# Performance work log

Hardware: AMD Instinct MI355X
Metric: run time of the kernel (lower is better)

Reference implementation:

```python
import jax, jax.numpy as jnp
import numpy as np

N_NODES = 100000
N_EDGES = 1600000
EMB = 128
N_LAYER = 5
X_DIM = 178
E_DIM = 18
BN_EPS = 1e-5


def setup_inputs() -> dict:
    key = jax.random.key(0)
    ks = jax.random.split(key, 20)
    s = 0.05  # weight scale
    inp = {}
    inp["x"] = jax.random.normal(ks[0], (N_NODES, X_DIM), jnp.float32)
    inp["edge_attr"] = jax.random.uniform(ks[1], (N_EDGES, E_DIM), jnp.float32)
    # input MLP (178 -> emb -> emb, LeakyReLU 0.1)
    inp["iw1"] = jax.random.normal(ks[2], (X_DIM, EMB), jnp.float32) * s
    inp["ib1"] = jax.random.normal(ks[3], (EMB,), jnp.float32) * s
    inp["iw2"] = jax.random.normal(ks[4], (EMB, EMB), jnp.float32) * s
    inp["ib2"] = jax.random.normal(ks[5], (EMB,), jnp.float32) * s
    # per-layer edge embedding MLP (18 -> emb -> emb, LeakyReLU 0.1)
    inp["ew1"] = jax.random.normal(ks[6], (N_LAYER, E_DIM, EMB), jnp.float32) * s
    inp["eb1"] = jax.random.normal(ks[7], (N_LAYER, EMB), jnp.float32) * s
    inp["ew2"] = jax.random.normal(ks[8], (N_LAYER, EMB, EMB), jnp.float32) * s
    inp["eb2"] = jax.random.normal(ks[9], (N_LAYER, EMB), jnp.float32) * s
    # per-layer GIN update MLP (emb -> 2emb -> emb, ReLU)
    inp["mw1"] = jax.random.normal(ks[10], (N_LAYER, EMB, 2 * EMB), jnp.float32) * s
    inp["mb1"] = jax.random.normal(ks[11], (N_LAYER, 2 * EMB), jnp.float32) * s
    inp["mw2"] = jax.random.normal(ks[12], (N_LAYER, 2 * EMB, EMB), jnp.float32) * s
    inp["mb2"] = jax.random.normal(ks[13], (N_LAYER, EMB), jnp.float32) * s
    # per-layer BatchNorm affine params
    inp["gamma"] = jnp.ones((N_LAYER, EMB), jnp.float32)
    inp["beta"] = jnp.zeros((N_LAYER, EMB), jnp.float32)
    inp["edge_index"] = jax.random.randint(ks[14], (2, N_EDGES), 0, N_NODES)
    return inp


def _leaky(v):
    return jnp.where(v > 0, v, 0.1 * v)


def reference(x, edge_attr, iw1, ib1, iw2, ib2, ew1, eb1, ew2, eb2,
              mw1, mb1, mw2, mb2, gamma, beta, edge_index):
    src = edge_index[0]  # x_j gathered from source nodes (PyG source_to_target)
    dst = edge_index[1]
    n = x.shape[0]

    # input node MLP with LeakyReLU(0.1)
    h = _leaky(x @ iw1 + ib1) @ iw2 + ib2  # [N, EMB]

    for l in range(N_LAYER):
        # edge embeddings for real edges: [E, EMB]
        ee = _leaky(edge_attr @ ew1[l] + eb1[l]) @ ew2[l] + eb2[l]
        # self-loop edges have zero edge_attr -> constant embedding vector [EMB]
        self_e = _leaky(eb1[l]) @ ew2[l] + eb2[l]
        # message = x_j + edge_emb; aggregate (add) at destination, plus self-loop term
        msg = h[src] + ee
        aggr = jax.ops.segment_sum(msg, dst, num_segments=n) + h + self_e
        # GIN update MLP (ReLU)
        hh = jnp.maximum(aggr @ mw1[l] + mb1[l], 0.0) @ mw2[l] + mb2[l]
        # BatchNorm1d (training mode: batch stats, biased variance)
        mean = hh.mean(axis=0)
        var = hh.var(axis=0)
        hh = (hh - mean) / jnp.sqrt(var + BN_EPS) * gamma[l] + beta[l]
        if l < N_LAYER - 1:
            hh = jnp.maximum(hh, 0.0)  # ReLU on all but last layer; dropout p=0 is a no-op
        h = hh

    return h  # JK == 'last'
```

## Files before the change

kernel.cpp:

```cpp
#include <hip/hip_runtime.h>
#include <hip/hip_bf16.h>
#include <cstdint>
#include <cstddef>

#define NNODES 100000
#define NEDGES 1600000
#define EMBD 128
#define NLAYER 5
#define XDIM 178
#define EDIM 18
#define BNEPS 1e-5f

typedef __attribute__((ext_vector_type(8))) short short8;
typedef __attribute__((ext_vector_type(8))) unsigned short ushort8;
typedef __attribute__((ext_vector_type(4))) float f32x4;

static __device__ __forceinline__ float leakyf(float v){ return v > 0.f ? v : 0.1f*v; }
static __device__ __forceinline__ unsigned short f2b(float v){
  __hip_bfloat16 b = __float2bfloat16(v);
  return *reinterpret_cast<unsigned short*>(&b);
}
static __device__ __forceinline__ float b2f(unsigned short u){
  __hip_bfloat16 b = *reinterpret_cast<__hip_bfloat16*>(&u);
  return __bfloat162float(b);
}

__global__ __launch_bounds__(256) void k_hist(const int* __restrict__ dst, int* __restrict__ cnt){
  int e = blockIdx.x*256 + threadIdx.x;
  if (e < NEDGES) atomicAdd(&cnt[dst[e]], 1);
}

__global__ __launch_bounds__(256) void k_scan1(const int* __restrict__ cnt, int* __restrict__ rowptr,
                                               int* __restrict__ bsum){
  __shared__ int s[256];
  int t = threadIdx.x, i = blockIdx.x*256 + t;
  int v = (i < NNODES) ? cnt[i] : 0;
  s[t] = v; __syncthreads();
  for (int off=1; off<256; off<<=1){
    int x = (t>=off) ? s[t-off] : 0; __syncthreads();
    s[t] += x; __syncthreads();
  }
  if (i < NNODES) rowptr[i+1] = s[t];
  if (t == 255) bsum[blockIdx.x] = s[t];
}

__global__ __launch_bounds__(512) void k_scan2(const int* __restrict__ bsum, int* __restrict__ boff, int nb){
  __shared__ int s[512];
  int t = threadIdx.x;
  int v = (t < nb) ? bsum[t] : 0;
  s[t] = v; __syncthreads();
  for (int off=1; off<512; off<<=1){
    int x = (t>=off) ? s[t-off] : 0; __syncthreads();
    s[t] += x; __syncthreads();
  }
  if (t < nb) boff[t] = s[t] - v;
}

__global__ __launch_bounds__(256) void k_scan3(int* __restrict__ rowptr, const int* __restrict__ boff){
  int i = blockIdx.x*256 + threadIdx.x;
  if (i < NNODES) rowptr[i+1] += boff[i>>8];
  if (i == 0) rowptr[0] = 0;
}

__global__ __launch_bounds__(256) void k_curcopy(const int* __restrict__ rowptr, int* __restrict__ cursor){
  int i = blockIdx.x*256 + threadIdx.x;
  if (i < NNODES) cursor[i] = rowptr[i];
}

__global__ __launch_bounds__(256) void k_fill_new(const int* __restrict__ src, const int* __restrict__ dst,
                                                  const float* __restrict__ ea, int* __restrict__ cursor,
                                                  int* __restrict__ srcp, unsigned short* __restrict__ eap24){
  int e = blockIdx.x*256 + threadIdx.x;
  if (e >= NEDGES) return;
  int pos = atomicAdd(&cursor[dst[e]], 1);
  srcp[pos] = src[e];
  const float* a = ea + (size_t)e*EDIM;
  ushort8 r0, r1, r2;
  #pragma unroll
  for (int k=0;k<8;++k)  r0[k] = f2b(a[k]);
  #pragma unroll
  for (int k=0;k<8;++k)  r1[k] = f2b(a[8+k]);
  #pragma unroll
  for (int k=0;k<8;++k)  r2[k] = 0;
  r2[0] = f2b(a[16]); r2[1] = f2b(a[17]);
  r2[2] = 0x3F80;
  unsigned short* o = eap24 + (size_t)pos*24;
  *reinterpret_cast<ushort8*>(o)      = r0;
  *reinterpret_cast<ushort8*>(o + 8)  = r1;
  *reinterpret_cast<ushort8*>(o + 16) = r2;
}

__global__ __launch_bounds__(256) void k_fill(const int* __restrict__ src, const int* __restrict__ dst,
                                              const float* __restrict__ ea, int* __restrict__ cursor,
                                              int* __restrict__ perm, int* __restrict__ srcp,
                                              float* __restrict__ eap){
  int e = blockIdx.x*256 + threadIdx.x;
  if (e >= NEDGES) return;
  int pos = atomicAdd(&cursor[dst[e]], 1);
  perm[pos] = e;
  srcp[pos] = src[e];
  if (eap){
    const float* a = ea + (size_t)e*EDIM;
    float* o = eap + (size_t)pos*EDIM;
    #pragma unroll
    for (int k=0;k<EDIM;++k) o[k] = a[k];
  }
}

__global__ __launch_bounds__(128) void k_selfe(const float* __restrict__ eb1, const float* __restrict__ ew2,
                                               const float* __restrict__ eb2, float* __restrict__ selfe){
  int l = blockIdx.x, c = threadIdx.x;
  const float* b1 = eb1 + l*EMBD;
  const float* w2 = ew2 + (size_t)l*EMBD*EMBD;
  float acc = eb2[l*EMBD + c];
  for (int j=0;j<EMBD;++j) acc += leakyf(b1[j]) * w2[j*EMBD + c];
  selfe[l*EMBD + c] = acc;
}

__global__ __launch_bounds__(256) void k_wc(const float* __restrict__ ew2, const float* __restrict__ mw1,
                                            float* __restrict__ wc){
  int idx = blockIdx.x*256 + threadIdx.x;
  int l = idx >> 15, rem = idx & 32767;
  int i = rem >> 8, n = rem & 255;
  const float* e = ew2 + (size_t)l*EMBD*EMBD + i*EMBD;
  const float* m = mw1 + (size_t)l*EMBD*2*EMBD + n;
  float acc = 0.f;
  #pragma unroll 4
  for (int j=0;j<EMBD;++j) acc += e[j]*m[(size_t)j*2*EMBD];
  wc[idx] = acc;
}

__global__ __launch_bounds__(256) void k_pack(const float* __restrict__ s1, int rows1,
                                              const float* __restrict__ s2, int Kreal,
                                              int Kpad, int N, __hip_bfloat16* __restrict__ out){
  int idx = blockIdx.x*256 + threadIdx.x;
  if (idx >= Kpad*N) return;
  int k = idx / N, n = idx - k*N;
  float v = 0.f;
  if (k < rows1) v = s1[(size_t)k*N + n];
  else if (k < Kreal) v = s2[(size_t)(k-rows1)*N + n];
  unsigned short hi = f2b(v);
  unsigned short lo = f2b(v - b2f(hi));
  size_t o = (size_t)(k>>5)*N*32 + (size_t)n*32 + (k&31);
  unsigned short* po = (unsigned short*)out;
  po[o] = hi;
  po[(size_t)Kpad*N + o] = lo;
}

__global__ __launch_bounds__(256) void k_edge_mfma(
    const float* __restrict__ h, const int* __restrict__ rowptr,
    const int* __restrict__ srcp, const unsigned short* __restrict__ eap24,
    const float* __restrict__ ew1l, const float* __restrict__ eb1l,
    const float* __restrict__ eb2l, const float* __restrict__ selfel,
    float* __restrict__ S1, float* __restrict__ base)
{
  int tid = threadIdx.x;
  int lane = tid & 63;
  int lr = lane & 15, kb = lane >> 4;
  int half = lane >> 5, li = lane & 31;
  int c4 = li*4;

  short8 bh[8], bl[8];
  #pragma unroll
  for (int nf=0; nf<8; ++nf){
    int col = nf*16 + lr;
    ushort8 hh8, ll8;
    #pragma unroll
    for (int j=0;j<8;++j){
      int k = kb*8 + j;
      float v = 0.f;
      if (k < EDIM) v = ew1l[k*EMBD + col];
      else if (k == EDIM) v = eb1l[col];
      unsigned short hi = f2b(v);
      hh8[j] = hi;
      ll8[j] = f2b(v - b2f(hi));
    }
    bh[nf] = *reinterpret_cast<short8*>(&hh8);
    bl[nf] = *reinterpret_cast<short8*>(&ll8);
  }
  float4 sf4 = *(const float4*)(selfel + c4);
  float4 e24 = *(const float4*)(eb2l + c4);

  int wid = blockIdx.x*4 + (tid>>6);
  const int NW = gridDim.x*4;
  for (int node = wid; node < NNODES; node += NW){
    int rs = rowptr[node], re = rowptr[node+1];
    float s1p[8];
    #pragma unroll
    for (int nf=0;nf<8;++nf) s1p[nf]=0.f;
    f32x4 bacc = (f32x4)0.f;

    for (int c0 = rs; c0 < re; c0 += 16){
      int cnt = re - c0;

      #pragma unroll
      for (int p=0;p<8;++p){
        int r = 2*p + half;
        int e = c0 + r; if (e > re-1) e = re-1;
        float m = (r < cnt) ? 1.f : 0.f;
        int sp = srcp[e];
        float4 hv = *(const float4*)(h + (size_t)sp*EMBD + c4);
        bacc[0] = fmaf(m, hv.x, bacc[0]);
        bacc[1] = fmaf(m, hv.y, bacc[1]);
        bacc[2] = fmaf(m, hv.z, bacc[2]);
        bacc[3] = fmaf(m, hv.w, bacc[3]);
      }

      int idx = c0 + lr; if (idx > re-1) idx = re-1;
      short8 af = (short8)0;
      if (kb < 3){
        ushort8 t = *reinterpret_cast<const ushort8*>(eap24 + (size_t)idx*24 + kb*8);
        af = *reinterpret_cast<short8*>(&t);
      }
      if (lr >= cnt) af = (short8)0;
      #pragma unroll
      for (int nf=0;nf<8;++nf){
        f32x4 acc = (f32x4)0.f;
        acc = __builtin_amdgcn_mfma_f32_16x16x32_bf16(af, bl[nf], acc, 0,0,0);
        acc = __builtin_amdgcn_mfma_f32_16x16x32_bf16(af, bh[nf], acc, 0,0,0);
        #pragma unroll
        for (int j=0;j<4;++j){
          float v = acc[j];
          s1p[nf] = fmaf(0.55f, v, s1p[nf]);
          s1p[nf] = fmaf(0.45f, fabsf(v), s1p[nf]);
        }
      }
    }

    #pragma unroll
    for (int nf=0;nf<8;++nf){
      float v = s1p[nf];
      v += __shfl_xor(v, 16);
      v += __shfl_xor(v, 32);
      s1p[nf] = v;
    }
    float va = s1p[0], vb = s1p[1];
    if (kb == 1){ va = s1p[2]; vb = s1p[3]; }
    if (kb == 2){ va = s1p[4]; vb = s1p[5]; }
    if (kb == 3){ va = s1p[6]; vb = s1p[7]; }
    S1[(size_t)node*EMBD + kb*32 + lr]      = va;
    S1[(size_t)node*EMBD + kb*32 + 16 + lr] = vb;

    #pragma unroll
    for (int j=0;j<4;++j) bacc[j] += __shfl_xor(bacc[j], 32);

    if (half == 0){
      float deg = (float)(re - rs);
      float4 hn = *(const float4*)(h + (size_t)node*EMBD + c4);
      float4 o;
      o.x = bacc[0] + hn.x + sf4.x + deg*e24.x;
      o.y = bacc[1] + hn.y + sf4.y + deg*e24.y;
      o.z = bacc[2] + hn.z + sf4.z + deg*e24.z;
      o.w = bacc[3] + hn.w + sf4.w + deg*e24.w;
      *(float4*)(base + (size_t)node*EMBD + c4) = o;
    }
  }
}

__global__ __launch_bounds__(256) void k_edge(
    const float* __restrict__ h, const int* __restrict__ rowptr,
    const int* __restrict__ perm, const int* __restrict__ srcp,
    const float* __restrict__ edge_attr, const float* __restrict__ eaperm,
    const float* __restrict__ ew1l, const float* __restrict__ eb1l,
    const float* __restrict__ eb2l, const float* __restrict__ selfel,
    float* __restrict__ S1, float* __restrict__ base)
{
  __shared__ float w1s[EDIM*EMBD];
  __shared__ float b1s[EMBD];
  int tid = threadIdx.x;
  for (int i = tid; i < EDIM*EMBD; i += 256) w1s[i] = ew1l[i];
  if (tid < EMBD) b1s[tid] = eb1l[tid];
  __syncthreads();
  int lane = tid & 63;
  int node = blockIdx.x*4 + (tid >> 6);
  if (node >= NNODES) return;
  int rs = rowptr[node], re = rowptr[node+1];
  int c0 = lane*2;
  float s1x=0.f, s1y=0.f, bx=0.f, by=0.f;
  for (int i = rs; i < re; ++i){
    int s = __builtin_amdgcn_readfirstlane(srcp[i]);
    const float* ea;
    if (eaperm){
      ea = eaperm + (size_t)__builtin_amdgcn_readfirstlane(i)*EDIM;
    } else {
      ea = edge_attr + (size_t)__builtin_amdgcn_readfirstlane(perm[i])*EDIM;
    }
    float2 hs = *(const float2*)(h + (size_t)s*EMBD + c0);
    bx += hs.x; by += hs.y;
    float d0 = b1s[c0], d1 = b1s[c0+1];
    #pragma unroll
    for (int k=0;k<EDIM;++k){
      float av = ea[k];
      d0 += av * w1s[k*EMBD + c0];
      d1 += av * w1s[k*EMBD + c0 + 1];
    }
    s1x += leakyf(d0); s1y += leakyf(d1);
  }
  float deg = (float)(re - rs);
  float2 hv = *(const float2*)(h + (size_t)node*EMBD + c0);
  *(float2*)(S1 + (size_t)node*EMBD + c0) = make_float2(s1x, s1y);
  float bvx = bx + hv.x + selfel[c0]   + deg*eb2l[c0];
  float bvy = by + hv.y + selfel[c0+1] + deg*eb2l[c0+1];
  *(float2*)(base + (size_t)node*EMBD + c0) = make_float2(bvx, bvy);
}

template<int BN, int WGM, int WGN, bool ALO, int ACT, bool STATS, bool OBF16, bool CONCAT, bool KCHK, bool ABF16>
__global__ __launch_bounds__(512) void k_mgemm(
    const float* __restrict__ Af, const float* __restrict__ A1,
    const __hip_bfloat16* __restrict__ Ab,
    int M, int Kreal, int Kpad, int lda,
    const __hip_bfloat16* __restrict__ Bp,
    const float* __restrict__ bias,
    float* __restrict__ Cf, __hip_bfloat16* __restrict__ Cb, int ldc,
    float* __restrict__ stats)
{
  static_assert(WGM*WGN == 8, "8 waves");
  constexpr int BM = 128;
  constexpr int MF = BM/(16*WGM);
  constexpr int NF = BN/(16*WGN);
  constexpr int LDS_ROW = 40;
  __shared__ __align__(16) unsigned short Ah[BM*LDS_ROW];
  __shared__ __align__(16) unsigned short Al[ALO ? BM*LDS_ROW : 8];
  __shared__ float ssum[STATS ? BN : 4];
  __shared__ float ssq [STATS ? BN : 4];

  int tid = threadIdx.x;
  int row0 = blockIdx.x*BM;
  int w = tid >> 6, lane = tid & 63;
  int wm = w / WGN, wn = w % WGN;
  int lr = lane & 15, kb = lane >> 4;
  int wrow = wm*MF*16, wcol = wn*NF*16;

  if (STATS && tid < BN){ ssum[tid] = 0.f; ssq[tid] = 0.f; }

  f32x4 acc[MF][NF];
  #pragma unroll
  for (int a=0;a<MF;++a)
    #pragma unroll
    for (int b=0;b<NF;++b) acc[a][b] = (f32x4)0.f;

  const size_t planeSz = (size_t)Kpad*BN;
  int sr = tid >> 2;
  int skq = (tid & 3)*8;
  int grow = row0 + sr;
  const int KS = Kpad >> 5;

  for (int ks = 0; ks < KS; ++ks){
    int k0 = ks << 5;
    int kg = k0 + skq;
    ushort8 hv, lv;
    if (ABF16){
      short8 raw = (short8)0;
      if (grow < M) raw = *reinterpret_cast<const short8*>((const unsigned short*)Ab + (size_t)grow*lda + kg);
      hv = *reinterpret_cast<ushort8*>(&raw);
    } else {
      float v[8];
      if (KCHK){
        #pragma unroll
        for (int i=0;i<8;++i)
          v[i] = (grow < M && kg+i < Kreal) ? Af[(size_t)grow*lda + kg + i] : 0.f;
      } else {
        const float* s;
        if (CONCAT) s = (kg < EMBD) ? (Af + (size_t)grow*lda + kg) : (A1 + (size_t)grow*lda + (kg - EMBD));
        else        s = Af + (size_t)grow*lda + kg;
        float4 p0 = make_float4(0,0,0,0), p1 = make_float4(0,0,0,0);
        if (grow < M){ p0 = *(const float4*)s; p1 = *(const float4*)(s+4); }
        v[0]=p0.x; v[1]=p0.y; v[2]=p0.z; v[3]=p0.w;
        v[4]=p1.x; v[5]=p1.y; v[6]=p1.z; v[7]=p1.w;
      }
      #pragma unroll
      for (int i=0;i<8;++i){
        unsigned short h16 = f2b(v[i]);
        hv[i] = h16;
        if (ALO) lv[i] = f2b(v[i] - b2f(h16));
      }
    }
    __syncthreads();
    *reinterpret_cast<ushort8*>(&Ah[sr*LDS_ROW + skq]) = hv;
    if (ALO && !ABF16) *reinterpret_cast<ushort8*>(&Al[sr*LDS_ROW + skq]) = lv;
    __syncthreads();

    short8 ah[MF], al[MF];
    #pragma unroll
    for (int mf=0; mf<MF; ++mf){
      int r = (wrow + mf*16 + lr)*LDS_ROW + kb*8;
      ah[mf] = *reinterpret_cast<const short8*>(&Ah[r]);
      if (ALO) al[mf] = *reinterpret_cast<const short8*>(&Al[r]);
    }
    const unsigned short* bb = (const unsigned short*)Bp + (size_t)ks*BN*32;
    short8 bh[NF], blv[NF];
    #pragma unroll
    for (int nf=0; nf<NF; ++nf){
      size_t off = (size_t)(wcol + nf*16 + lr)*32 + kb*8;
      bh[nf] = *reinterpret_cast<const short8*>(bb + off);
      blv[nf] = *reinterpret_cast<const short8*>(bb + planeSz + off);
    }
    #pragma unroll
    for (int mf=0; mf<MF; ++mf){
      #pragma unroll
      for (int nf=0; nf<NF; ++nf){
        acc[mf][nf] = __builtin_amdgcn_mfma_f32_16x16x32_bf16(ah[mf], bh[nf], acc[mf][nf], 0, 0, 0);
        acc[mf][nf] = __builtin_amdgcn_mfma_f32_16x16x32_bf16(ah[mf], blv[nf], acc[mf][nf], 0, 0, 0);
        if (ALO)
          acc[mf][nf] = __builtin_amdgcn_mfma_f32_16x16x32_bf16(al[mf], bh[nf], acc[mf][nf], 0, 0, 0);
      }
    }
  }

  float bcol[NF];
  #pragma unroll
  for (int nf=0; nf<NF; ++nf) bcol[nf] = bias ? bias[wcol + nf*16 + lr] : 0.f;
  float s[NF], sq[NF];
  #pragma unroll
  for (int nf=0; nf<NF; ++nf){ s[nf]=0.f; sq[nf]=0.f; }

  #pragma unroll
  for (int mf=0; mf<MF; ++mf){
    #pragma unroll
    for (int j=0; j<4; ++j){
      int r = row0 + wrow + mf*16 + kb*4 + j;
      if (r < M){
        #pragma unroll
        for (int nf=0; nf<NF; ++nf){
          int c = wcol + nf*16 + lr;
          float v = acc[mf][nf][j] + bcol[nf];
          if (ACT == 1) v = leakyf(v);
          if (ACT == 2) v = fmaxf(v, 0.f);
          if (OBF16) Cb[(size_t)r*ldc + c] = __float2bfloat16(v);
          else       Cf[(size_t)r*ldc + c] = v;
          if (STATS){ s[nf] += v; sq[nf] += v*v; }
        }
      }
    }
  }
  if (STATS){
    #pragma unroll
    for (int nf=0; nf<NF; ++nf){
      atomicAdd(&ssum[wcol + nf*16 + lr], s[nf]);
      atomicAdd(&ssq [wcol + nf*16 + lr], sq[nf]);
    }
    __syncthreads();
    if (tid < BN){
      atomicAdd(&stats[tid], ssum[tid]);
      atomicAdd(&stats[BN + tid], ssq[tid]);
    }
  }
}

__global__ __launch_bounds__(256) void k_bn(const float* __restrict__ hh, const float* __restrict__ stats,
                                            const float* __restrict__ gamma, const float* __restrict__ beta,
                                            float* __restrict__ out, int dorelu){
  int idx = blockIdx.x*256 + threadIdx.x;
  if (idx >= NNODES*(EMBD/4)) return;
  int c0 = (idx & (EMBD/4 - 1)) * 4;
  float4 v = *(const float4*)(hh + (size_t)idx*4);
  float o[4] = {v.x, v.y, v.z, v.w};
  const float invN = 1.f / (float)NNODES;
  #pragma unroll
  for (int i=0;i<4;++i){
    int c = c0 + i;
    float mean = stats[c] * invN;
    float var  = stats[EMBD + c] * invN - mean*mean;
    float inv  = rsqrtf(fmaxf(var, 0.f) + BNEPS);
    float y = (o[i] - mean) * inv * gamma[c] + beta[c];
    if (dorelu) y = fmaxf(y, 0.f);
    o[i] = y;
  }
  *(float4*)(out + (size_t)idx*4) = make_float4(o[0],o[1],o[2],o[3]);
}

extern "C" void kernel_launch(void* const* d_in, const int* in_sizes, int n_in,
                              void* d_out, int out_size, void* d_ws, size_t ws_size,
                              hipStream_t stream)
{
  const float* x   = (const float*)d_in[0];
  const float* ea  = (const float*)d_in[1];
  const float* iw1 = (const float*)d_in[2];
  const float* ib1 = (const float*)d_in[3];
  const float* iw2 = (const float*)d_in[4];
  const float* ib2 = (const float*)d_in[5];
  const float* ew1 = (const float*)d_in[6];
  const float* eb1 = (const float*)d_in[7];
  const float* ew2 = (const float*)d_in[8];
  const float* eb2 = (const float*)d_in[9];
  const float* mw1 = (const float*)d_in[10];
  const float* mb1 = (const float*)d_in[11];
  const float* mw2 = (const float*)d_in[12];
  const float* mb2 = (const float*)d_in[13];
  const float* gamma = (const float*)d_in[14];
  const float* beta  = (const float*)d_in[15];
  const int* eidx = (const int*)d_in[16];
  const int* srcI = eidx;
  const int* dstI = eidx + NEDGES;

  char* p = (char*)d_ws;
  auto alloc = [&](size_t bytes)->char*{
    char* r = p; p += (bytes + 255) & ~(size_t)255; return r;
  };
  float* hbuf  = (float*)alloc((size_t)NNODES*EMBD*4);
  float* S1    = (float*)alloc((size_t)NNODES*EMBD*4);
  float* base  = (float*)alloc((size_t)NNODES*EMBD*4);
  __hip_bfloat16* tbuf = (__hip_bfloat16*)alloc((size_t)NNODES*2*EMBD*2);
  int* perm   = (int*)alloc((size_t)NEDGES*4);
  int* srcp   = (int*)alloc((size_t)NEDGES*4);
  int* rowptr = (int*)alloc((size_t)(NNODES+1)*4);
  int* cursor = (int*)alloc((size_t)NNODES*4);
  int* bsum   = (int*)alloc(4096);
  int* boff   = (int*)alloc(4096);
  float* selfe = (float*)alloc(NLAYER*EMBD*4);
  float* stats = (float*)alloc(2*EMBD*4);
  float* wc    = (float*)alloc((size_t)NLAYER*EMBD*2*EMBD*4);
  __hip_bfloat16* Bi1 = (__hip_bfloat16*)alloc((size_t)192*EMBD*2*2);
  __hip_bfloat16* Bi2 = (__hip_bfloat16*)alloc((size_t)EMBD*EMBD*2*2);
  __hip_bfloat16* B1  = (__hip_bfloat16*)alloc((size_t)NLAYER*256*256*2*2);
  __hip_bfloat16* B2  = (__hip_bfloat16*)alloc((size_t)NLAYER*256*EMBD*2*2);
  size_t used = (size_t)(p - (char*)d_ws);

  bool use_new = (ws_size >= used + (size_t)NEDGES*24*2 + 256);
  unsigned short* eap24 = nullptr;
  float* eaperm = nullptr;
  if (use_new) eap24 = (unsigned short*)alloc((size_t)NEDGES*24*2);
  else if (ws_size >= used + (size_t)NEDGES*EDIM*4 + 256)
    eaperm = (float*)alloc((size_t)NEDGES*EDIM*4);

  hipMemsetAsync(cursor, 0, (size_t)NNODES*4, stream);
  k_hist<<<(NEDGES+255)/256, 256, 0, stream>>>(dstI, cursor);
  int nb = (NNODES+255)/256;
  k_scan1<<<nb, 256, 0, stream>>>(cursor, rowptr, bsum);
  k_scan2<<<1, 512, 0, stream>>>(bsum, boff, nb);
  k_scan3<<<(NNODES+255)/256, 256, 0, stream>>>(rowptr, boff);
  k_curcopy<<<(NNODES+255)/256, 256, 0, stream>>>(rowptr, cursor);
  if (use_new)
    k_fill_new<<<(NEDGES+255)/256, 256, 0, stream>>>(srcI, dstI, ea, cursor, srcp, eap24);
  else
    k_fill<<<(NEDGES+255)/256, 256, 0, stream>>>(srcI, dstI, ea, cursor, perm, srcp, eaperm);
  k_selfe<<<NLAYER, EMBD, 0, stream>>>(eb1, ew2, eb2, selfe);

  k_wc<<<(NLAYER*EMBD*2*EMBD)/256, 256, 0, stream>>>(ew2, mw1, wc);
  k_pack<<<(192*EMBD+255)/256, 256, 0, stream>>>(iw1, XDIM, iw1, XDIM, 192, EMBD, Bi1);
  k_pack<<<(EMBD*EMBD+255)/256, 256, 0, stream>>>(iw2, EMBD, iw2, EMBD, EMBD, EMBD, Bi2);
  for (int l=0; l<NLAYER; ++l){
    k_pack<<<(256*256+255)/256, 256, 0, stream>>>(
        wc + (size_t)l*EMBD*2*EMBD, EMBD, mw1 + (size_t)l*EMBD*2*EMBD, 256, 256, 256,
        B1 + (size_t)l*256*256*2);
    k_pack<<<(256*EMBD+255)/256, 256, 0, stream>>>(
        mw2 + (size_t)l*2*EMBD*EMBD, 256, mw2, 256, 256, EMBD,
        B2 + (size_t)l*256*EMBD*2);
  }

  const int gx = (NNODES + 127)/128;

  k_mgemm<128,4,2, true,1,false,false,false,true ,false><<<gx, 512, 0, stream>>>(
      x, nullptr, nullptr, NNODES, XDIM, 192, XDIM, Bi1, ib1, S1, nullptr, EMBD, nullptr);
  k_mgemm<128,4,2, true,0,false,false,false,false,false><<<gx, 512, 0, stream>>>(
      S1, nullptr, nullptr, NNODES, EMBD, EMBD, EMBD, Bi2, ib2, hbuf, nullptr, EMBD, nullptr);

  for (int l=0; l<NLAYER; ++l){
    hipMemsetAsync(stats, 0, 2*EMBD*4, stream);
    if (use_new)
      k_edge_mfma<<<1536, 256, 0, stream>>>(
          hbuf, rowptr, srcp, eap24,
          ew1 + (size_t)l*EDIM*EMBD, eb1 + l*EMBD, eb2 + l*EMBD, selfe + l*EMBD,
          S1, base);
    else
      k_edge<<<NNODES/4, 256, 0, stream>>>(
          hbuf, rowptr, perm, srcp, ea, eaperm,
          ew1 + (size_t)l*EDIM*EMBD, eb1 + l*EMBD, eb2 + l*EMBD, selfe + l*EMBD,
          S1, base);
    k_mgemm<256,2,4, true,2,false,true ,true ,false,false><<<gx, 512, 0, stream>>>(
        S1, base, nullptr, NNODES, 256, 256, EMBD, B1 + (size_t)l*256*256*2,
        mb1 + l*2*EMBD, nullptr, tbuf, 2*EMBD, nullptr);
    k_mgemm<128,4,2, false,0,true ,false,false,false,true ><<<gx, 512, 0, stream>>>(
        nullptr, nullptr, tbuf, NNODES, 256, 256, 2*EMBD, B2 + (size_t)l*256*EMBD*2,
        mb2 + l*EMBD, S1, nullptr, EMBD, stats);
    float* outp = (l == NLAYER-1) ? (float*)d_out : hbuf;
    k_bn<<<(NNODES*(EMBD/4)+255)/256, 256, 0, stream>>>(
        S1, stats, gamma + l*EMBD, beta + l*EMBD, outp, (l < NLAYER-1) ? 1 : 0);
  }
}
```

Measured before the change: 2.078 ms.

## Split fused edge kernel into separate gather and MFMA S1 kernels

The fused per-node edge kernel is split in two. One kernel does the neighbor-feature gather and writes the base aggregate, using 32-lane slots per node. The other does only the MFMA-based edge-embedding nonlinearity sum into S1. Separating them lets each kernel use its own mapping and register budget, and can improve occupancy for the memory-bound gather. The cost is an extra launch and a second pass over rowptr.

Result: slower. 2.239 ms (+7.7%).

```diff
diff --git a/kernel.cpp b/kernel.cpp
--- a/kernel.cpp
+++ b/kernel.cpp
@@ -147,18 +147,55 @@
   po[(size_t)Kpad*N + o] = lo;
 }
 
-__global__ __launch_bounds__(256) void k_edge_mfma(
+__global__ __launch_bounds__(256) void k_gather(
     const float* __restrict__ h, const int* __restrict__ rowptr,
-    const int* __restrict__ srcp, const unsigned short* __restrict__ eap24,
+    const int* __restrict__ srcp,
+    const float* __restrict__ eb2l, const float* __restrict__ selfel,
+    float* __restrict__ base)
+{
+  int tid = threadIdx.x;
+  int li = tid & 31;
+  int c4 = li*4;
+  float4 sf4 = *(const float4*)(selfel + c4);
+  float4 e24 = *(const float4*)(eb2l + c4);
+  int slot = blockIdx.x*8 + (tid>>5);
+  const int NS = gridDim.x*8;
+  for (int node = slot; node < NNODES; node += NS){
+    int rs = rowptr[node], re = rowptr[node+1];
+    f32x4 b = (f32x4)0.f;
+    for (int c0 = rs; c0 < re; c0 += 8){
+      int cnt = re - c0;
+      #pragma unroll
+      for (int p=0;p<8;++p){
+        int e = c0 + p; if (e > re-1) e = re-1;
+        float m = (p < cnt) ? 1.f : 0.f;
+        int sp = srcp[e];
+        float4 hv = *(const float4*)(h + (size_t)sp*EMBD + c4);
+        b[0] = fmaf(m, hv.x, b[0]);
+        b[1] = fmaf(m, hv.y, b[1]);
+        b[2] = fmaf(m, hv.z, b[2]);
+        b[3] = fmaf(m, hv.w, b[3]);
+      }
+    }
+    float deg = (float)(re - rs);
+    float4 hn = *(const float4*)(h + (size_t)node*EMBD + c4);
+    float4 o;
+    o.x = b[0] + hn.x + sf4.x + deg*e24.x;
+    o.y = b[1] + hn.y + sf4.y + deg*e24.y;
+    o.z = b[2] + hn.z + sf4.z + deg*e24.z;
+    o.w = b[3] + hn.w + sf4.w + deg*e24.w;
+    *(float4*)(base + (size_t)node*EMBD + c4) = o;
+  }
+}
+
+__global__ __launch_bounds__(256) void k_s1(
+    const int* __restrict__ rowptr, const unsigned short* __restrict__ eap24,
     const float* __restrict__ ew1l, const float* __restrict__ eb1l,
-    const float* __restrict__ eb2l, const float* __restrict__ selfel,
-    float* __restrict__ S1, float* __restrict__ base)
+    float* __restrict__ S1)
 {
   int tid = threadIdx.x;
   int lane = tid & 63;
   int lr = lane & 15, kb = lane >> 4;
-  int half = lane >> 5, li = lane & 31;
-  int c4 = li*4;
 
   short8 bh[8], bl[8];
   #pragma unroll
@@ -178,8 +215,6 @@
     bh[nf] = *reinterpret_cast<short8*>(&hh8);
     bl[nf] = *reinterpret_cast<short8*>(&ll8);
   }
-  float4 sf4 = *(const float4*)(selfel + c4);
-  float4 e24 = *(const float4*)(eb2l + c4);
 
   int wid = blockIdx.x*4 + (tid>>6);
   const int NW = gridDim.x*4;
@@ -188,24 +223,9 @@
     float s1p[8];
     #pragma unroll
     for (int nf=0;nf<8;++nf) s1p[nf]=0.f;
-    f32x4 bacc = (f32x4)0.f;
 
     for (int c0 = rs; c0 < re; c0 += 16){
       int cnt = re - c0;
-
-      #pragma unroll
-      for (int p=0;p<8;++p){
-        int r = 2*p + half;
-        int e = c0 + r; if (e > re-1) e = re-1;
-        float m = (r < cnt) ? 1.f : 0.f;
-        int sp = srcp[e];
-        float4 hv = *(const float4*)(h + (size_t)sp*EMBD + c4);
-        bacc[0] = fmaf(m, hv.x, bacc[0]);
-        bacc[1] = fmaf(m, hv.y, bacc[1]);
-        bacc[2] = fmaf(m, hv.z, bacc[2]);
-        bacc[3] = fmaf(m, hv.w, bacc[3]);
-      }
-
       int idx = c0 + lr; if (idx > re-1) idx = re-1;
       short8 af = (short8)0;
       if (kb < 3){
@@ -240,20 +260,6 @@
     if (kb == 3){ va = s1p[6]; vb = s1p[7]; }
     S1[(size_t)node*EMBD + kb*32 + lr]      = va;
     S1[(size_t)node*EMBD + kb*32 + 16 + lr] = vb;
-
-    #pragma unroll
-    for (int j=0;j<4;++j) bacc[j] += __shfl_xor(bacc[j], 32);
-
-    if (half == 0){
-      float deg = (float)(re - rs);
-      float4 hn = *(const float4*)(h + (size_t)node*EMBD + c4);
-      float4 o;
-      o.x = bacc[0] + hn.x + sf4.x + deg*e24.x;
-      o.y = bacc[1] + hn.y + sf4.y + deg*e24.y;
-      o.z = bacc[2] + hn.z + sf4.z + deg*e24.z;
-      o.w = bacc[3] + hn.w + sf4.w + deg*e24.w;
-      *(float4*)(base + (size_t)node*EMBD + c4) = o;
-    }
   }
 }
 
@@ -557,16 +563,17 @@
 
   for (int l=0; l<NLAYER; ++l){
     hipMemsetAsync(stats, 0, 2*EMBD*4, stream);
-    if (use_new)
-      k_edge_mfma<<<1536, 256, 0, stream>>>(
-          hbuf, rowptr, srcp, eap24,
-          ew1 + (size_t)l*EDIM*EMBD, eb1 + l*EMBD, eb2 + l*EMBD, selfe + l*EMBD,
-          S1, base);
-    else
+    if (use_new){
+      k_gather<<<2048, 256, 0, stream>>>(
+          hbuf, rowptr, srcp, eb2 + l*EMBD, selfe + l*EMBD, base);
+      k_s1<<<2048, 256, 0, stream>>>(
+          rowptr, eap24, ew1 + (size_t)l*EDIM*EMBD, eb1 + l*EMBD, S1);
+    } else {
       k_edge<<<NNODES/4, 256, 0, stream>>>(
           hbuf, rowptr, perm, srcp, ea, eaperm,
           ew1 + (size_t)l*EDIM*EMBD, eb1 + l*EMBD, eb2 + l*EMBD, selfe + l*EMBD,
           S1, base);
+    }
     k_mgemm<256,2,4, true,2,false,true ,true ,false,false><<<gx, 512, 0, stream>>>(
         S1, base, nullptr, NNODES, 256, 256, EMBD, B1 + (size_t)l*256*256*2,
         mb1 + l*2*EMBD, nullptr, tbuf, 2*EMBD, nullptr);
```
